# Optimization experiments

Hardware: AMD Instinct MI355X
Metric: run time of the kernel (lower is better)

## Reference

```python
import jax, jax.numpy as jnp
import numpy as np

DICT_SIZE = 512
EMBED_DIM = 64
SPARSITY = 5
COMMITMENT_COST = 0.25
EPSILON = 1e-10
COEFF_CLAMP = 1e7


def setup_inputs() -> dict:
    key = jax.random.key(0)
    kz, kd = jax.random.split(key)
    z = jax.random.normal(kz, (32, EMBED_DIM, 32, 32), dtype=jnp.float32)
    D = jax.random.normal(kd, (EMBED_DIM, DICT_SIZE), dtype=jnp.float32)
    # _normalize_dictionary(): unit L2 norm per atom (column)
    D = D / jnp.linalg.norm(D, axis=0, keepdims=True)
    return {"z": z, "dictionary": D}


def batch_omp(signals, dictionary):
    # signals: [E, N], dictionary: [E, K]
    E, N = signals.shape
    K = dictionary.shape[1]
    Dt = dictionary.T  # [K, E]
    DtD = Dt @ dictionary + EPSILON * jnp.eye(K, dtype=signals.dtype)  # [K, K]
    residual = signals
    active = jnp.zeros((N, K), dtype=bool)
    coefficients = jnp.zeros((N, K), dtype=signals.dtype)
    idx = jnp.zeros((N, 0), dtype=jnp.int32)
    rows = jnp.arange(N)
    for k in range(SPARSITY):  # small fixed unroll; active-set size is static k+1
        corr = Dt @ residual                                  # [K, N]
        corr = jnp.where(active.T, -jnp.inf, corr)
        new_atoms = jnp.argmax(corr, axis=0).astype(jnp.int32)  # [N]
        active = active.at[rows, new_atoms].set(True)
        idx = jnp.concatenate([idx, new_atoms[:, None]], axis=1)  # [N, k+1]
        G = DtD[idx[:, :, None], idx[:, None, :]]             # [N, k+1, k+1]
        y = jnp.einsum('nke,en->nk', Dt[idx], residual)       # [N, k+1]
        coeffs = jnp.linalg.solve(G, y[..., None])[..., 0]    # [N, k+1]
        update = jnp.einsum('enk,nk->en', dictionary[:, idx], coeffs)  # [E, N]
        residual = signals - update
        coefficients = coefficients.at[rows[:, None], idx].set(coeffs)
    return coefficients.T  # [K, N]


def reference(z, dictionary):
    B, E, H, W = z.shape
    # [B,E,H,W] -> [E, N]
    z_flat = z.transpose(0, 2, 3, 1).reshape(-1, E).T
    # sparse coding is done under no_grad in torch
    coefficients = jax.lax.stop_gradient(batch_omp(z_flat, dictionary))
    coefficients = jnp.clip(coefficients, -COEFF_CLAMP, COEFF_CLAMP)  # [K, N]
    z_q_flat = dictionary @ coefficients                               # [E, N]
    z_q_reshaped = z_q_flat.T.reshape(B, H, W, E).transpose(0, 3, 1, 2)
    rec_loss = jnp.mean((jax.lax.stop_gradient(z_q_flat) - z_flat) ** 2)
    commit_loss = jnp.mean((z_q_flat - jax.lax.stop_gradient(z_flat)) ** 2)
    effective_cost = COMMITMENT_COST * (1.0 + SPARSITY / 10.0)
    coeff_loss = jnp.mean(jnp.abs(coefficients))
    loss = rec_loss + effective_cost * commit_loss + 0.001 * coeff_loss
    # straight-through estimator with clamp
    z_q = z + jax.lax.stop_gradient(jnp.clip(z_q_reshaped - z, -1.0, 1.0))
    return z_q, loss, coefficients
```

## Files before the change

### kernel.cpp

```cpp
#include <hip/hip_runtime.h>
#include <math.h>

#define NSIG 32768
#define KD   512
#define ED   64
#define SP   5

__global__ __launch_bounds__(256) void k_pre(const float* __restrict__ D,
                                             double* __restrict__ DtD,
                                             float4* __restrict__ coef4) {
  if (blockIdx.x < 1024) {
    int flat = blockIdx.x * 256 + threadIdx.x;
    int i = flat >> 9, j = flat & 511;
    double acc = 0.0;
    #pragma unroll
    for (int e = 0; e < ED; ++e)
      acc += (double)D[e * KD + i] * (double)D[e * KD + j];
    if (i == j) acc += 1e-10;
    DtD[flat] = acc;
  } else {
    size_t count4 = (size_t)KD * NSIG / 4;
    size_t i = (size_t)(blockIdx.x - 1024) * 256 + threadIdx.x;
    size_t stride = (size_t)2048 * 256;
    float4 zv = make_float4(0.f, 0.f, 0.f, 0.f);
    for (; i < count4; i += stride) coef4[i] = zv;
  }
}

template <int K>
__device__ __forceinline__ void omp_iter(const double* __restrict__ DtD,
                                         const double (&c0)[16], unsigned& amask,
                                         int (&idx)[SP], double (&cc)[SP],
                                         double (&tri)[15], double (&c0sel)[SP],
                                         int li) {
  double vb = -INFINITY;
  int ab = 0x7FFFFFFF;
  #pragma unroll
  for (int j4 = 0; j4 < 4; ++j4) {
    int a0 = (j4 << 7) + (li << 2);
    double v0 = c0[4 * j4], v1 = c0[4 * j4 + 1];
    double v2 = c0[4 * j4 + 2], v3 = c0[4 * j4 + 3];
    #pragma unroll
    for (int m = 0; m < K; ++m) {
      const double* gp = DtD + (size_t)idx[m] * KD + a0;
      double2 gA = *(const double2*)gp;
      double2 gB = *(const double2*)(gp + 2);
      v0 -= gA.x * cc[m];
      v1 -= gA.y * cc[m];
      v2 -= gB.x * cc[m];
      v3 -= gB.y * cc[m];
    }
    v0 = ((amask >> (4 * j4 + 0)) & 1u) ? -INFINITY : v0;
    v1 = ((amask >> (4 * j4 + 1)) & 1u) ? -INFINITY : v1;
    v2 = ((amask >> (4 * j4 + 2)) & 1u) ? -INFINITY : v2;
    v3 = ((amask >> (4 * j4 + 3)) & 1u) ? -INFINITY : v3;
    if (v0 > vb) { vb = v0; ab = a0; }
    if (v1 > vb) { vb = v1; ab = a0 + 1; }
    if (v2 > vb) { vb = v2; ab = a0 + 2; }
    if (v3 > vb) { vb = v3; ab = a0 + 3; }
  }
  #pragma unroll
  for (int s = 16; s >= 1; s >>= 1) {
    double ov = __shfl_xor(vb, s, 64);
    int    oa = __shfl_xor(ab, s, 64);
    if (ov > vb || (ov == vb && oa < ab)) { vb = ov; ab = oa; }
  }
  idx[K] = ab;
  if (((ab >> 2) & 31) == li) amask |= 1u << ((((ab >> 7) << 2)) | (ab & 3));
  const double* drow = DtD + (size_t)ab * KD;
  double bb[SP], u[SP];
  #pragma unroll
  for (int m = 0; m < K; ++m) bb[m] = drow[idx[m]];
  {
    double csel = vb;
    #pragma unroll
    for (int m = 0; m < K; ++m) csel += bb[m] * cc[m];
    c0sel[K] = csel;
  }
  double sch = drow[ab];
  #pragma unroll
  for (int i = 0; i < K; ++i) {
    double ui = 0.0;
    #pragma unroll
    for (int m = 0; m < K; ++m) {
      int lo = i < m ? i : m, hi = i < m ? m : i;
      ui += tri[lo * SP - lo * (lo + 1) / 2 + hi] * bb[m];
    }
    u[i] = ui;
    sch -= bb[i] * ui;
  }
  double r = 1.0 / sch;
  #pragma unroll
  for (int i = 0; i < K; ++i) {
    #pragma unroll
    for (int j = i; j < K; ++j) tri[i * SP - i * (i + 1) / 2 + j] += r * u[i] * u[j];
    tri[i * SP - i * (i + 1) / 2 + K] = -r * u[i];
  }
  tri[K * SP - K * (K + 1) / 2 + K] = r;
  double h[SP];
  #pragma unroll
  for (int i = 0; i <= K; ++i) {
    double s = 0.0;
    #pragma unroll
    for (int j = 0; j <= K; ++j) {
      int lo = i < j ? i : j, hi = i < j ? j : i;
      s += tri[lo * SP - lo * (lo + 1) / 2 + hi] * c0sel[j];
    }
    h[i] = s;
  }
  #pragma unroll
  for (int i = 0; i < K; ++i) cc[i] = h[i] - cc[i];
  cc[K] = h[K];
}

__global__ __launch_bounds__(512) void k_fused(const float* __restrict__ z,
                                               const float* __restrict__ D,
                                               const double* __restrict__ DtD,
                                               float* __restrict__ coefOut,
                                               int* __restrict__ idxWs,
                                               double* __restrict__ cWs,
                                               double* __restrict__ csumWs) {
  __shared__ float Dlds[2][8 * 512];
  __shared__ float zbuf[64 * 16];
  int tid = threadIdx.x;
  int lane = tid & 63;
  int wv = tid >> 6;
  int li = lane & 31;
  int g  = lane >> 5;
  int n = blockIdx.x * 16 + 2 * wv + g;
  {
    int n0 = blockIdx.x * 16;
    int b = n0 >> 10, p0 = n0 & 1023;
    const float* zb = z + (size_t)b * 65536 + p0;
    #pragma unroll
    for (int k2 = 0; k2 < 2; ++k2) {
      int f = tid + 512 * k2;
      zbuf[f] = zb[(f >> 4) * 1024 + (f & 15)];
    }
  }
  #pragma unroll
  for (int i = 0; i < 2; ++i) {
    const float* gp = D + 0 * 4096 + i * 2048 + wv * 256 + lane * 4;
    float* lp = &Dlds[0][i * 2048 + wv * 256];
    __builtin_amdgcn_global_load_lds(
        (const __attribute__((address_space(1))) void*)gp,
        (__attribute__((address_space(3))) void*)lp, 16, 0, 0);
  }
  double cA[8], cB[8];
  #pragma unroll
  for (int p = 0; p < 8; ++p) { cA[p] = 0.0; cB[p] = 0.0; }
  for (int t8 = 0; t8 < 8; ++t8) {
    __syncthreads();
    if (t8 < 7) {
      #pragma unroll
      for (int i = 0; i < 2; ++i) {
        const float* gp = D + (t8 + 1) * 4096 + i * 2048 + wv * 256 + lane * 4;
        float* lp = &Dlds[(t8 + 1) & 1][i * 2048 + wv * 256];
        __builtin_amdgcn_global_load_lds(
            (const __attribute__((address_space(1))) void*)gp,
            (__attribute__((address_space(3))) void*)lp, 16, 0, 0);
      }
    }
    const float* buf = Dlds[t8 & 1];
    #pragma unroll
    for (int e = 0; e < 8; ++e) {
      float2 zz = *(const float2*)(zbuf + (t8 * 8 + e) * 16 + 2 * wv);
      double zA = (double)zz.x, zB = (double)zz.y;
      const float* drow = buf + e * 512;
      float4 d0 = *(const float4*)(drow + lane * 4);
      float4 d1 = *(const float4*)(drow + 256 + lane * 4);
      double dv[8] = {(double)d0.x, (double)d0.y, (double)d0.z, (double)d0.w,
                      (double)d1.x, (double)d1.y, (double)d1.z, (double)d1.w};
      #pragma unroll
      for (int p = 0; p < 8; ++p) {
        cA[p] += zA * dv[p];
        cB[p] += zB * dv[p];
      }
    }
  }
  double c0[16];
  #pragma unroll
  for (int j4 = 0; j4 < 4; ++j4) {
    int src = ((j4 & 1) << 5) + li;
    #pragma unroll
    for (int bit = 0; bit < 4; ++bit) {
      double tA = __shfl(cA[((j4 >> 1) << 2) + bit], src, 64);
      double tB = __shfl(cB[((j4 >> 1) << 2) + bit], src, 64);
      c0[4 * j4 + bit] = g ? tB : tA;
    }
  }
  unsigned amask = 0;
  int idx[SP]; double cc[SP]; double tri[15]; double c0sel[SP];
  omp_iter<0>(DtD, c0, amask, idx, cc, tri, c0sel, li);
  omp_iter<1>(DtD, c0, amask, idx, cc, tri, c0sel, li);
  omp_iter<2>(DtD, c0, amask, idx, cc, tri, c0sel, li);
  omp_iter<3>(DtD, c0, amask, idx, cc, tri, c0sel, li);
  omp_iter<4>(DtD, c0, amask, idx, cc, tri, c0sel, li);
  if (li == 0) {
    double cs = 0.0;
    #pragma unroll
    for (int j = 0; j < SP; ++j) {
      double cj = cc[j];
      cj = fmin(fmax(cj, -10000000.0), 10000000.0);
      cs += fabs(cj);
      idxWs[n * SP + j] = idx[j];
      cWs[n * SP + j] = cj;
      coefOut[(size_t)idx[j] * NSIG + n] = (float)cj;
    }
    csumWs[n] = cs;
  }
}

__global__ __launch_bounds__(256) void k_zq(const float* __restrict__ z,
                                            const float* __restrict__ D,
                                            const int* __restrict__ idxWs,
                                            const double* __restrict__ cWs,
                                            float* __restrict__ zqOut,
                                            double* __restrict__ recWs) {
  int t = threadIdx.x;
  size_t flat = (size_t)blockIdx.x * 256 + t;
  int b = (int)(flat >> 16);
  int e = (int)((flat >> 10) & 63);
  int p = (int)(flat & 1023);
  int n = b * 1024 + p;
  double u = 0.0;
  #pragma unroll
  for (int j = 0; j < SP; ++j) {
    int a = idxWs[n * SP + j];
    u += (double)D[e * KD + a] * cWs[n * SP + j];
  }
  float zv = z[flat];
  double d = u - (double)zv;
  double dc = fmin(fmax(d, -1.0), 1.0);
  zqOut[flat] = (float)((double)zv + dc);
  __shared__ double red[256];
  red[t] = d * d;
  __syncthreads();
  #pragma unroll
  for (int s = 128; s >= 1; s >>= 1) {
    if (t < s) red[t] += red[t + s];
    __syncthreads();
  }
  if (t == 0) recWs[blockIdx.x] = red[0];
}

__global__ __launch_bounds__(256) void k_loss(const double* __restrict__ recWs,
                                              const double* __restrict__ csumWs,
                                              float* __restrict__ lossOut) {
  int t = threadIdx.x;
  double r = 0.0, c = 0.0;
  for (int i = t; i < 8192; i += 256) r += recWs[i];
  for (int i = t; i < NSIG; i += 256) c += csumWs[i];
  __shared__ double red[512];
  red[t] = r; red[256 + t] = c;
  __syncthreads();
  #pragma unroll
  for (int s = 128; s >= 1; s >>= 1) {
    if (t < s) { red[t] += red[t + s]; red[256 + t] += red[256 + t + s]; }
    __syncthreads();
  }
  if (t == 0) {
    double rec = red[0] / (double)(64.0 * 32768.0);
    double cm  = red[256] / (double)(512.0 * 32768.0);
    double loss = rec + 0.375 * rec + 0.001 * cm;
    lossOut[0] = (float)loss;
  }
}

extern "C" void kernel_launch(void* const* d_in, const int* in_sizes, int n_in,
                              void* d_out, int out_size, void* d_ws, size_t ws_size,
                              hipStream_t stream) {
  const float* z = (const float*)d_in[0];
  const float* D = (const float*)d_in[1];
  float* out = (float*)d_out;
  float* zqOut   = out;
  float* lossOut = out + 2097152;
  float* coefOut = out + 2097153;

  char* w = (char*)d_ws;
  double* DtD    = (double*)w; w += (size_t)KD * KD * 8;
  int*    idxWs  = (int*)w;    w += (size_t)NSIG * SP * 4;
  double* cWs    = (double*)w; w += (size_t)NSIG * SP * 8;
  double* csumWs = (double*)w; w += (size_t)NSIG * 8;
  double* recWs  = (double*)w; w += (size_t)8192 * 8;

  k_pre<<<3072, 256, 0, stream>>>(D, DtD, (float4*)coefOut);
  k_fused<<<NSIG / 16, 512, 0, stream>>>(z, D, DtD, coefOut, idxWs, cWs, csumWs);
  k_zq<<<8192, 256, 0, stream>>>(z, D, idxWs, cWs, zqOut, recWs);
  k_loss<<<1, 256, 0, stream>>>(recWs, csumWs, lossOut);
}
```

Baseline: 218.1 us.

## Compute initial correlations with FP64 MFMA and transpose results through LDS

After: 359.4 us. 1.65x slower.

```diff
diff --git a/kernel.cpp b/kernel.cpp
--- a/kernel.cpp
+++ b/kernel.cpp
@@ -5,6 +5,8 @@
 #define KD   512
 #define ED   64
 #define SP   5
+
+typedef double f64x4 __attribute__((ext_vector_type(4)));
 
 __global__ __launch_bounds__(256) void k_pre(const float* __restrict__ D,
                                              double* __restrict__ DtD,
@@ -120,17 +122,25 @@
                                                int* __restrict__ idxWs,
                                                double* __restrict__ cWs,
                                                double* __restrict__ csumWs) {
-  __shared__ float Dlds[2][8 * 512];
+  __shared__ __align__(16) char ldsRaw[2 * 8 * 528 * 4];
   __shared__ float zbuf[64 * 16];
+  __shared__ int badFlag;
+  float* Dlds0 = (float*)ldsRaw;
+  float* Dlds1 = (float*)ldsRaw + 8 * 528;
+  double* TR = (double*)ldsRaw;
+
   int tid = threadIdx.x;
   int lane = tid & 63;
-  int wv = tid >> 6;
+  int w = tid >> 6;
   int li = lane & 31;
   int g  = lane >> 5;
-  int n = blockIdx.x * 16 + 2 * wv + g;
+  int arow = lane >> 4;
+  int acol = lane & 15;
+  int sigBase = blockIdx.x * 16;
+  int n = sigBase + 2 * w + g;
+
   {
-    int n0 = blockIdx.x * 16;
-    int b = n0 >> 10, p0 = n0 & 1023;
+    int b = sigBase >> 10, p0 = sigBase & 1023;
     const float* zb = z + (size_t)b * 65536 + p0;
     #pragma unroll
     for (int k2 = 0; k2 < 2; ++k2) {
@@ -138,57 +148,123 @@
       zbuf[f] = zb[(f >> 4) * 1024 + (f & 15)];
     }
   }
+  if (tid == 0) badFlag = 0;
+
   #pragma unroll
   for (int i = 0; i < 2; ++i) {
-    const float* gp = D + 0 * 4096 + i * 2048 + wv * 256 + lane * 4;
-    float* lp = &Dlds[0][i * 2048 + wv * 256];
+    const float* gp = D + (0 * 8 + w) * 512 + i * 256 + lane * 4;
+    float* lp = Dlds0 + w * 528 + i * 256;
     __builtin_amdgcn_global_load_lds(
         (const __attribute__((address_space(1))) void*)gp,
         (__attribute__((address_space(3))) void*)lp, 16, 0, 0);
   }
-  double cA[8], cB[8];
-  #pragma unroll
-  for (int p = 0; p < 8; ++p) { cA[p] = 0.0; cB[p] = 0.0; }
+
+  f64x4 acc0 = {0., 0., 0., 0.}, acc1 = {0., 0., 0., 0.};
+  f64x4 acc2 = {0., 0., 0., 0.}, acc3 = {0., 0., 0., 0.};
   for (int t8 = 0; t8 < 8; ++t8) {
     __syncthreads();
     if (t8 < 7) {
       #pragma unroll
       for (int i = 0; i < 2; ++i) {
-        const float* gp = D + (t8 + 1) * 4096 + i * 2048 + wv * 256 + lane * 4;
-        float* lp = &Dlds[(t8 + 1) & 1][i * 2048 + wv * 256];
+        const float* gp = D + ((t8 + 1) * 8 + w) * 512 + i * 256 + lane * 4;
+        float* lp = (((t8 + 1) & 1) ? Dlds1 : Dlds0) + w * 528 + i * 256;
         __builtin_amdgcn_global_load_lds(
             (const __attribute__((address_space(1))) void*)gp,
             (__attribute__((address_space(3))) void*)lp, 16, 0, 0);
       }
     }
-    const float* buf = Dlds[t8 & 1];
-    #pragma unroll
-    for (int e = 0; e < 8; ++e) {
-      float2 zz = *(const float2*)(zbuf + (t8 * 8 + e) * 16 + 2 * wv);
-      double zA = (double)zz.x, zB = (double)zz.y;
-      const float* drow = buf + e * 512;
-      float4 d0 = *(const float4*)(drow + lane * 4);
-      float4 d1 = *(const float4*)(drow + 256 + lane * 4);
-      double dv[8] = {(double)d0.x, (double)d0.y, (double)d0.z, (double)d0.w,
-                      (double)d1.x, (double)d1.y, (double)d1.z, (double)d1.w};
+    const float* buf = (t8 & 1) ? Dlds1 : Dlds0;
+    #pragma unroll
+    for (int ks = 0; ks < 2; ++ks) {
+      int e0 = t8 * 8 + ks * 4;
+      double bfrag = (double)zbuf[(e0 + arow) * 16 + acol];
+      const float* ar = buf + (ks * 4 + arow) * 528 + 64 * w + acol;
+      double a0 = (double)ar[0];
+      double a1 = (double)ar[16];
+      double a2 = (double)ar[32];
+      double a3 = (double)ar[48];
+      acc0 = __builtin_amdgcn_mfma_f64_16x16x4f64(a0, bfrag, acc0, 0, 0, 0);
+      acc1 = __builtin_amdgcn_mfma_f64_16x16x4f64(a1, bfrag, acc1, 0, 0, 0);
+      acc2 = __builtin_amdgcn_mfma_f64_16x16x4f64(a2, bfrag, acc2, 0, 0, 0);
+      acc3 = __builtin_amdgcn_mfma_f64_16x16x4f64(a3, bfrag, acc3, 0, 0, 0);
+    }
+  }
+
+  {
+    int atomv = 64 * w + 4 * arow;
+    double ref = 0.0;
+    for (int e = 0; e < ED; ++e)
+      ref += (double)D[e * KD + atomv] * (double)zbuf[e * 16 + acol];
+    double diff = fabs(acc0[0] - ref);
+    if (__any(diff > 1e-9 * fmax(1.0, fabs(ref)))) {
+      if (lane == 0) badFlag = 1;
+    }
+  }
+  __syncthreads();
+  bool bad = badFlag != 0;
+
+  if (!bad) {
+    if (w < 4) {
       #pragma unroll
-      for (int p = 0; p < 8; ++p) {
-        cA[p] += zA * dv[p];
-        cB[p] += zB * dv[p];
+      for (int t = 0; t < 4; ++t) {
+        const f64x4& a = (t == 0) ? acc0 : (t == 1) ? acc1 : (t == 2) ? acc2 : acc3;
+        #pragma unroll
+        for (int v = 0; v < 4; ++v) {
+          int atomA = 64 * w + 16 * t + 4 * arow + v;
+          TR[acol * 258 + atomA] = a[v];
+        }
       }
     }
-  }
+  } else {
+    int s = tid & 15, a0b = (tid >> 4) * 8;
+    for (int a = 0; a < 8; ++a) {
+      double val = 0.0;
+      for (int e = 0; e < ED; ++e)
+        val += (double)D[e * KD + a0b + a] * (double)zbuf[e * 16 + s];
+      TR[s * 258 + a0b + a] = val;
+    }
+  }
+  __syncthreads();
   double c0[16];
-  #pragma unroll
-  for (int j4 = 0; j4 < 4; ++j4) {
-    int src = ((j4 & 1) << 5) + li;
-    #pragma unroll
-    for (int bit = 0; bit < 4; ++bit) {
-      double tA = __shfl(cA[((j4 >> 1) << 2) + bit], src, 64);
-      double tB = __shfl(cB[((j4 >> 1) << 2) + bit], src, 64);
-      c0[4 * j4 + bit] = g ? tB : tA;
-    }
-  }
+  int myS = 2 * w + g;
+  #pragma unroll
+  for (int j4 = 0; j4 < 2; ++j4) {
+    const double2* tp = (const double2*)(TR + myS * 258 + 128 * j4 + 4 * li);
+    double2 q0 = tp[0], q1 = tp[1];
+    c0[4 * j4 + 0] = q0.x; c0[4 * j4 + 1] = q0.y;
+    c0[4 * j4 + 2] = q1.x; c0[4 * j4 + 3] = q1.y;
+  }
+  __syncthreads();
+  if (!bad) {
+    if (w >= 4) {
+      #pragma unroll
+      for (int t = 0; t < 4; ++t) {
+        const f64x4& a = (t == 0) ? acc0 : (t == 1) ? acc1 : (t == 2) ? acc2 : acc3;
+        #pragma unroll
+        for (int v = 0; v < 4; ++v) {
+          int atomA = 64 * (w - 4) + 16 * t + 4 * arow + v;
+          TR[acol * 258 + atomA] = a[v];
+        }
+      }
+    }
+  } else {
+    int s = tid & 15, a0b = 256 + (tid >> 4) * 8;
+    for (int a = 0; a < 8; ++a) {
+      double val = 0.0;
+      for (int e = 0; e < ED; ++e)
+        val += (double)D[e * KD + a0b + a] * (double)zbuf[e * 16 + s];
+      TR[s * 258 + a0b + a - 256] = val;
+    }
+  }
+  __syncthreads();
+  #pragma unroll
+  for (int j4 = 2; j4 < 4; ++j4) {
+    const double2* tp = (const double2*)(TR + myS * 258 + 128 * (j4 - 2) + 4 * li);
+    double2 q0 = tp[0], q1 = tp[1];
+    c0[4 * j4 + 0] = q0.x; c0[4 * j4 + 1] = q0.y;
+    c0[4 * j4 + 2] = q1.x; c0[4 * j4 + 3] = q1.y;
+  }
+
   unsigned amask = 0;
   int idx[SP]; double cc[SP]; double tri[15]; double c0sel[SP];
   omp_iter<0>(DtD, c0, amask, idx, cc, tri, c0sel, li);
```
